# Kernel tuning notes

Hardware: AMD Instinct MI355X
Metric: run time of the kernel (lower is better)

Reference implementation:

```python
import jax, jax.numpy as jnp
import numpy as np


def _hann_filter(P):
    # ramp filter built in spatial domain (Kak & Slaney) times fftshifted Hann window
    n = np.concatenate([np.arange(1, P // 2 + 1, 2), np.arange(P // 2 - 1, 0, -2)]).astype(np.float64)
    f = np.zeros(P, np.float64)
    f[0] = 0.25
    f[1::2] = -1.0 / (np.pi * n) ** 2
    ramp = 2.0 * np.real(np.fft.fft(f))
    filt = ramp * np.fft.fftshift(np.hanning(P))
    return jnp.asarray(filt, jnp.float32)


def _fbp(sino, angles, circle):
    B, A, L = sino.shape
    P = max(64, int(2 ** np.ceil(np.log2(2 * L))))  # img_size_padded
    center = L // 2
    # --- FFT filtering (filtered=True) ---
    filt = _hann_filter(P)
    sino_p = jnp.pad(sino, ((0, 0), (0, 0), (0, P - L)))
    sino_f = jnp.real(jnp.fft.ifft(jnp.fft.fft(sino_p, axis=-1) * filt, axis=-1))[:, :, :L]
    # --- back-projection: emulate grid_sample(bilinear, align_corners=True, padding zeros) ---
    x, y = jnp.meshgrid(jnp.arange(L, dtype=jnp.float32) - center,
                        jnp.arange(L, dtype=jnp.float32) - center, indexing='ij')
    th = angles + jnp.pi / 2
    t = x[None] * jnp.cos(th)[:, None, None] + y[None] * jnp.sin(th)[:, None, None]  # [A,L,L]
    # t_norm = 2t/(L-1); align_corners pixel coord = (t_norm+1)/2*(L-1) = t + (L-1)/2
    u = t + (L - 1) / 2.0
    i0 = jnp.floor(u)
    frac = u - i0
    i0i = i0.astype(jnp.int32)
    i1i = i0i + 1
    v0 = (i0i >= 0) & (i0i < L)
    v1 = (i1i >= 0) & (i1i < L)
    w0 = jnp.where(v0, 1.0 - frac, 0.0)  # zero-padding: kill OOB taps
    w1 = jnp.where(v1, frac, 0.0)
    aidx = jnp.arange(A)[:, None, None]
    g0 = sino_f[:, aidx, jnp.clip(i0i, 0, L - 1)]  # [B,A,L,L]
    g1 = sino_f[:, aidx, jnp.clip(i1i, 0, L - 1)]
    recon = jnp.sum(w0[None] * g0 + w1[None] * g1, axis=1)  # [B,L,L]
    if circle:
        Y, X = np.ogrid[:L, :L]
        mask = jnp.asarray(np.sqrt((X - center) ** 2 + (Y - center) ** 2) > center)
        recon = jnp.where(mask[None], 0.0, recon)
    return recon


def setup_inputs() -> dict:
    key = jax.random.key(0)
    sino = jax.random.normal(key, (2, 181, 512), dtype=jnp.float32)
    angles = jnp.linspace(0.0, np.pi, 181).astype(jnp.float32)
    return {"sino": sino, "angles": angles, "circle": 1}


def reference(sino, angles, circle):
    return _fbp(sino, angles, circle)
```

## Files before the change

kernel.cpp:

```cpp
#include <hip/hip_runtime.h>
#include <math.h>

#define OFF_FILT 0
#define OFF_HR   1024
#define OFF_CTH  2048
#define OFF_STH  2304
#define OFF_SF   4096

#define PAD   108
#define ROWE  728
#define CHUNK 8

__device__ __forceinline__ float cos2pi(float x) {
  return __builtin_amdgcn_cosf(x);
}

__global__ __launch_bounds__(256) void k_filt(const float* __restrict__ angles,
                                              float* __restrict__ ws) {
  const int t = threadIdx.x & 63;
  const int k = blockIdx.x * 4 + (threadIdx.x >> 6);
  float acc = 0.f;
#pragma unroll
  for (int q = 0; q < 8; q++) {
    int tt = t + 64 * q;
    int n = (tt < 256) ? (2 * tt + 1) : (1023 - 2 * tt);
    float pin = 3.14159265358979f * (float)n;
    float cf = -1.0f / (pin * pin);
    int r = ((2 * tt + 1) * k) & 1023;
    acc = fmaf(cf, cos2pi((float)r * (1.0f / 1024.0f)), acc);
  }
#pragma unroll
  for (int o = 32; o; o >>= 1) acc += __shfl_down(acc, o, 64);
  if (t == 0) {
    float ramp = 0.5f + 2.0f * acc;
    int ks = (k + 512) & 1023;
    float hann = 0.5f - 0.5f * cos2pi((float)ks * (1.0f / 1023.0f));
    ws[OFF_FILT + k] = ramp * hann;
  }
  if (blockIdx.x == 0 && threadIdx.x < 181) {
    float th = angles[threadIdx.x] + 1.5707963267948966f;
    ws[OFF_CTH + threadIdx.x] = cosf(th);
    ws[OFF_STH + threadIdx.x] = sinf(th);
  }
}

__global__ __launch_bounds__(256) void k_hr(float* __restrict__ ws) {
  const int t = threadIdx.x & 63;
  const int m = blockIdx.x * 4 + (threadIdx.x >> 6);
  float acc = 0.f;
  int r = (t * m) & 1023;
  const int step = (64 * m) & 1023;
#pragma unroll
  for (int q = 0; q < 16; q++) {
    acc = fmaf(ws[OFF_FILT + t + 64 * q],
               cos2pi((float)r * (1.0f / 1024.0f)), acc);
    r = (r + step) & 1023;
  }
#pragma unroll
  for (int o = 32; o; o >>= 1) acc += __shfl_down(acc, o, 64);
  if (t == 0) ws[OFF_HR + m] = acc * (1.0f / 1024.0f);
}

__global__ __launch_bounds__(512) void k_conv(const float* __restrict__ sino,
                                              float* __restrict__ ws) {
  __shared__ float smem[6144];
  const int tid = threadIdx.x;
  const int a = blockIdx.x >> 1;
  const int half = blockIdx.x & 1;
  const int lane = tid & 63;
  float* s_s0 = smem;
  float* s_s1 = smem + 512;
  float* s_hr = smem + 1024;
  float* part = smem + 2048;
  if (tid < 128) {
    ((float4*)s_s0)[tid] = ((const float4*)(sino + (size_t)a * 512))[tid];
  } else if (tid < 256) {
    ((float4*)s_s1)[tid - 128] =
        ((const float4*)(sino + (size_t)(181 + a) * 512))[tid - 128];
  } else {
    ((float4*)s_hr)[tid - 256] = ((const float4*)(ws + OFF_HR))[tid - 256];
  }
  __syncthreads();

  const int w = tid >> 6;
  const int base = half * 256 + lane * 4;
  float acc0[4] = {0.f, 0.f, 0.f, 0.f};
  float acc1[4] = {0.f, 0.f, 0.f, 0.f};
  const float4* SH = (const float4*)s_hr;
  const float4* S0 = (const float4*)s_s0;
  const float4* S1 = (const float4*)s_s1;
#pragma unroll
  for (int ii = 0; ii < 8; ii++) {
    const int j8 = w * 64 + ii * 8;
    float4 sa0 = S0[j8 >> 2];
    float4 sb0 = S0[(j8 >> 2) + 1];
    float4 sa1 = S1[j8 >> 2];
    float4 sb1 = S1[(j8 >> 2) + 1];
    int wi = base - j8;
    float4 h0 = SH[((wi - 8) & 1023) >> 2];
    float4 h1 = SH[((wi - 4) & 1023) >> 2];
    float4 h2 = SH[(wi & 1023) >> 2];
    float qq[12] = {h0.x, h0.y, h0.z, h0.w, h1.x, h1.y,
                    h1.z, h1.w, h2.x, h2.y, h2.z, h2.w};
    float v0[8] = {sa0.x, sa0.y, sa0.z, sa0.w, sb0.x, sb0.y, sb0.z, sb0.w};
    float v1[8] = {sa1.x, sa1.y, sa1.z, sa1.w, sb1.x, sb1.y, sb1.z, sb1.w};
#pragma unroll
    for (int jj = 0; jj < 8; jj++) {
#pragma unroll
      for (int m = 0; m < 4; m++) {
        acc0[m] = fmaf(v0[jj], qq[8 + m - jj], acc0[m]);
        acc1[m] = fmaf(v1[jj], qq[8 + m - jj], acc1[m]);
      }
    }
  }
  float* pw = part + w * 512 + lane * 8;
  ((float4*)pw)[0] = make_float4(acc0[0], acc1[0], acc0[1], acc1[1]);
  ((float4*)pw)[1] = make_float4(acc0[2], acc1[2], acc0[3], acc1[3]);
  __syncthreads();
  float s = part[tid];
#pragma unroll
  for (int ww = 1; ww < 8; ww++) s += part[ww * 512 + tid];
  ws[OFF_SF + (size_t)a * 1024 + half * 512 + tid] = s;
}

__global__ __launch_bounds__(1024) void k_bp(const float* __restrict__ ws,
                                             const int* __restrict__ circ,
                                             float* __restrict__ out) {
  __shared__ float2 srow[CHUNK * ROWE];
  const int tid = threadIdx.x;
  const int j = tid & 511;
  const int ir = tid >> 9;
  const int i = blockIdx.x * 2 + ir;
  const float xc = (float)(i - 256);
  const float yc = (float)(j - 256);
  const float* __restrict__ cth = ws + OFF_CTH;
  const float* __restrict__ sth = ws + OFF_STH;
  float acc0 = 0.f, acc1 = 0.f;

  const int circv = circ[0];
  const int dx = j - 256, dy = i - 256;
  const bool msk = (circv != 0) && (dx * dx + dy * dy > 65536);
  const bool wskip = (__all((int)msk) != 0);

  const float2 z2 = make_float2(0.f, 0.f);
  if (tid < PAD) {
#pragma unroll
    for (int r = 0; r < CHUNK; r++) srow[r * ROWE + tid] = z2;
  }
  if (tid < ROWE - PAD - 512) {
#pragma unroll
    for (int r = 0; r < CHUNK; r++) srow[r * ROWE + PAD + 512 + tid] = z2;
  }

  const int r0 = tid >> 8, r1 = r0 + 4;
  const int col = tid & 255;
  const float4* __restrict__ G = (const float4*)(ws + OFF_SF);
  float4* SW0 = (float4*)&srow[r0 * ROWE + PAD + col * 2];
  float4* SW1 = (float4*)&srow[r1 * ROWE + PAD + col * 2];
  const int rowcap = 180;

  int A = 0;
  float4 pre0 = G[min(r0, rowcap) * 256 + col];
  float4 pre1 = G[min(r1, rowcap) * 256 + col];

  for (int c = 0; c < 23; c++) {
    __syncthreads();
    *SW0 = pre0;
    *SW1 = pre1;
    const int An = A + CHUNK;
    if (c < 22) {
      pre0 = G[min(An + r0, rowcap) * 256 + col];
      pre1 = G[min(An + r1, rowcap) * 256 + col];
    }
    __syncthreads();
    if (!wskip) {
      const int nv = min(CHUNK, 181 - A);
#pragma unroll
      for (int r = 0; r < CHUNK; r++) {
        if (r >= nv) break;
        const int a = A + r;
        const float c_ = cth[a];
        const float s_ = sth[a];
        float u = fmaf(xc, c_, fmaf(yc, s_, 255.5f + (float)PAD));
        int b = (int)u;
        float fr = __builtin_amdgcn_fractf(u);
        const float2* rp = &srow[r * ROWE];
        float2 t0 = rp[b];
        float2 t1 = rp[b + 1];
        float w0 = 1.0f - fr;
        acc0 = fmaf(w0, t0.x, fmaf(fr, t1.x, acc0));
        acc1 = fmaf(w0, t0.y, fmaf(fr, t1.y, acc1));
      }
    }
    A = An;
  }
  const size_t o = (size_t)i * 512 + j;
  out[o] = msk ? 0.f : acc0;
  out[262144 + o] = msk ? 0.f : acc1;
}

extern "C" void kernel_launch(void* const* d_in, const int* in_sizes, int n_in,
                              void* d_out, int out_size, void* d_ws, size_t ws_size,
                              hipStream_t stream) {
  const float* sino = (const float*)d_in[0];
  const float* angles = (const float*)d_in[1];
  const int* circ = (const int*)d_in[2];
  float* ws = (float*)d_ws;
  float* out = (float*)d_out;

  hipLaunchKernelGGL(k_filt, dim3(256), dim3(256),  0, stream, angles, ws);
  hipLaunchKernelGGL(k_hr,   dim3(256), dim3(256),  0, stream, ws);
  hipLaunchKernelGGL(k_conv, dim3(362), dim3(512),  0, stream, sino, ws);
  hipLaunchKernelGGL(k_bp,   dim3(256), dim3(1024), 0, stream, ws, circ, out);
}
```

Measured before the change: 88.83 us.

## Double-buffer backprojection rows via direct global-to-LDS loads and pack cos/sin

```diff
diff --git a/kernel.cpp b/kernel.cpp
--- a/kernel.cpp
+++ b/kernel.cpp
@@ -3,16 +3,23 @@
 
 #define OFF_FILT 0
 #define OFF_HR   1024
-#define OFF_CTH  2048
-#define OFF_STH  2304
+#define OFF_CS   2048
 #define OFF_SF   4096
 
 #define PAD   108
 #define ROWE  728
 #define CHUNK 8
+#define HALFE (CHUNK * ROWE)
 
 __device__ __forceinline__ float cos2pi(float x) {
   return __builtin_amdgcn_cosf(x);
+}
+
+typedef unsigned int u32;
+__device__ __forceinline__ void gload_lds16(const void* g, void* l) {
+  __builtin_amdgcn_global_load_lds(
+      (const __attribute__((address_space(1))) u32*)g,
+      (__attribute__((address_space(3))) u32*)l, 16, 0, 0);
 }
 
 __global__ __launch_bounds__(256) void k_filt(const float* __restrict__ angles,
@@ -39,8 +46,8 @@
   }
   if (blockIdx.x == 0 && threadIdx.x < 181) {
     float th = angles[threadIdx.x] + 1.5707963267948966f;
-    ws[OFF_CTH + threadIdx.x] = cosf(th);
-    ws[OFF_STH + threadIdx.x] = sinf(th);
+    ws[OFF_CS + 2 * threadIdx.x]     = cosf(th);
+    ws[OFF_CS + 2 * threadIdx.x + 1] = sinf(th);
   }
 }
 
@@ -126,15 +133,14 @@
 __global__ __launch_bounds__(1024) void k_bp(const float* __restrict__ ws,
                                              const int* __restrict__ circ,
                                              float* __restrict__ out) {
-  __shared__ float2 srow[CHUNK * ROWE];
+  __shared__ float2 srow[2 * HALFE];
   const int tid = threadIdx.x;
   const int j = tid & 511;
   const int ir = tid >> 9;
   const int i = blockIdx.x * 2 + ir;
   const float xc = (float)(i - 256);
   const float yc = (float)(j - 256);
-  const float* __restrict__ cth = ws + OFF_CTH;
-  const float* __restrict__ sth = ws + OFF_STH;
+  const float2* __restrict__ CS = (const float2*)(ws + OFF_CS);
   float acc0 = 0.f, acc1 = 0.f;
 
   const int circv = circ[0];
@@ -145,46 +151,43 @@
   const float2 z2 = make_float2(0.f, 0.f);
   if (tid < PAD) {
 #pragma unroll
-    for (int r = 0; r < CHUNK; r++) srow[r * ROWE + tid] = z2;
+    for (int r = 0; r < 2 * CHUNK; r++) srow[r * ROWE + tid] = z2;
   }
   if (tid < ROWE - PAD - 512) {
 #pragma unroll
-    for (int r = 0; r < CHUNK; r++) srow[r * ROWE + PAD + 512 + tid] = z2;
-  }
-
-  const int r0 = tid >> 8, r1 = r0 + 4;
+    for (int r = 0; r < 2 * CHUNK; r++) srow[r * ROWE + PAD + 512 + tid] = z2;
+  }
+
+  const int r0 = tid >> 8;
   const int col = tid & 255;
-  const float4* __restrict__ G = (const float4*)(ws + OFF_SF);
-  float4* SW0 = (float4*)&srow[r0 * ROWE + PAD + col * 2];
-  float4* SW1 = (float4*)&srow[r1 * ROWE + PAD + col * 2];
-  const int rowcap = 180;
+  const float4* __restrict__ G4 = (const float4*)(ws + OFF_SF);
+  float2* L0 = &srow[r0 * ROWE + PAD + col * 2];
+  float2* L1 = L0 + 4 * ROWE;
+
+  gload_lds16(&G4[min(r0, 180) * 256 + col], L0);
+  gload_lds16(&G4[min(r0 + 4, 180) * 256 + col], L1);
+  __syncthreads();
 
   int A = 0;
-  float4 pre0 = G[min(r0, rowcap) * 256 + col];
-  float4 pre1 = G[min(r1, rowcap) * 256 + col];
-
   for (int c = 0; c < 23; c++) {
-    __syncthreads();
-    *SW0 = pre0;
-    *SW1 = pre1;
-    const int An = A + CHUNK;
+    const int cur = c & 1;
     if (c < 22) {
-      pre0 = G[min(An + r0, rowcap) * 256 + col];
-      pre1 = G[min(An + r1, rowcap) * 256 + col];
+      const int An = A + CHUNK;
+      const int doff = cur ? 0 : HALFE;
+      gload_lds16(&G4[min(An + r0, 180) * 256 + col], L0 + doff);
+      gload_lds16(&G4[min(An + r0 + 4, 180) * 256 + col], L1 + doff);
     }
-    __syncthreads();
     if (!wskip) {
       const int nv = min(CHUNK, 181 - A);
+      const float2* __restrict__ rb = srow + cur * HALFE;
 #pragma unroll
       for (int r = 0; r < CHUNK; r++) {
         if (r >= nv) break;
-        const int a = A + r;
-        const float c_ = cth[a];
-        const float s_ = sth[a];
-        float u = fmaf(xc, c_, fmaf(yc, s_, 255.5f + (float)PAD));
+        const float2 cs = CS[A + r];
+        float u = fmaf(xc, cs.x, fmaf(yc, cs.y, 255.5f + (float)PAD));
         int b = (int)u;
         float fr = __builtin_amdgcn_fractf(u);
-        const float2* rp = &srow[r * ROWE];
+        const float2* rp = rb + r * ROWE;
         float2 t0 = rp[b];
         float2 t1 = rp[b + 1];
         float w0 = 1.0f - fr;
@@ -192,7 +195,8 @@
         acc1 = fmaf(w0, t0.y, fmaf(fr, t1.y, acc1));
       }
     }
-    A = An;
+    __syncthreads();
+    A += CHUNK;
   }
   const size_t o = (size_t)i * 512 + j;
   out[o] = msk ? 0.f : acc0;
```

Measured after the change: 95.75 us. +7.8%, slower.
